# Performance work log

Hardware: AMD Instinct MI355X
Metric: run time of the kernel (lower is better)

Reference implementation:

```python
import jax, jax.numpy as jnp
import numpy as np

B, H, F, E, K = 32, 4096, 4096, 8, 2

def setup_inputs() -> dict:
    key = jax.random.key(0)
    ks = jax.random.split(key, 5)
    x = jax.random.normal(ks[0], (B, H), dtype=jnp.float32)
    Wg = jax.random.normal(ks[1], (H, E), dtype=jnp.float32) * 0.02
    W1 = jax.random.normal(ks[2], (E, H, F), dtype=jnp.float32) * 0.02
    W3 = jax.random.normal(ks[3], (E, H, F), dtype=jnp.float32) * 0.02
    W2 = jax.random.normal(ks[4], (E, F, H), dtype=jnp.float32) * 0.02
    return {"x": x, "Wg": Wg, "W1": W1, "W3": W3, "W2": W2}

def reference(x, Wg, W1, W3, W2):
    # Gate: [B, E] logits, top-2 selection, softmax over the 2 selected logits
    logits = x @ Wg                                   # [B, E]
    vals, idx = jax.lax.top_k(logits, K)              # [B, K]
    w = jax.nn.softmax(vals, axis=-1)                 # [B, K]
    # Combine weights per expert: [B, E] (zero for unselected experts)
    combine = jnp.sum(jax.nn.one_hot(idx, E, dtype=x.dtype) * w[..., None], axis=1)
    h = jnp.einsum('bh,ehf->ebf', x, W1)              # [E, B, F]
    g = jax.nn.silu(h) * jnp.einsum('bh,ehf->ebf', x, W3)
    y = jnp.einsum('ebf,efh->ebh', g, W2)             # [E, B, H]
    # Scatter-combine: weighted sum over experts (all-gather + reduce-sum in source)
    return jnp.einsum('be,ebh->bh', combine, y)       # [B, H]
```

## Files before the change

kernel.cpp:

```cpp
#include <hip/hip_runtime.h>
#include <cstdint>

#define BB 32
#define HH 4096
#define FF 4096
#define EE 8
#define NSLOT 16
#define TSEG 16
#define CH 512
#define RSTR 36

__global__ __launch_bounds__(256) void gate_kernel(const float* __restrict__ x,
                                                   const float* __restrict__ Wg,
                                                   float* __restrict__ logits) {
  int b = blockIdx.x;
  int tid = threadIdx.x;
  float acc[EE];
#pragma unroll
  for (int e = 0; e < EE; ++e) acc[e] = 0.f;
  const float* xb = x + (size_t)b * HH;
  for (int h = tid; h < HH; h += 256) {
    float xv = xb[h];
    const float4* wg = (const float4*)(Wg + (size_t)h * EE);
    float4 w0 = wg[0], w1 = wg[1];
    acc[0] = fmaf(xv, w0.x, acc[0]);
    acc[1] = fmaf(xv, w0.y, acc[1]);
    acc[2] = fmaf(xv, w0.z, acc[2]);
    acc[3] = fmaf(xv, w0.w, acc[3]);
    acc[4] = fmaf(xv, w1.x, acc[4]);
    acc[5] = fmaf(xv, w1.y, acc[5]);
    acc[6] = fmaf(xv, w1.z, acc[6]);
    acc[7] = fmaf(xv, w1.w, acc[7]);
  }
#pragma unroll
  for (int off = 32; off > 0; off >>= 1) {
#pragma unroll
    for (int e = 0; e < EE; ++e) acc[e] += __shfl_down(acc[e], off, 64);
  }
  __shared__ float part[4][EE];
  if ((tid & 63) == 0) {
#pragma unroll
    for (int e = 0; e < EE; ++e) part[tid >> 6][e] = acc[e];
  }
  __syncthreads();
  if (tid < EE) {
    logits[(size_t)b * EE + tid] =
        part[0][tid] + part[1][tid] + part[2][tid] + part[3][tid];
  }
}

__global__ void route_kernel(const float* __restrict__ logits,
                             int* __restrict__ cnt,
                             int* __restrict__ tok,
                             float* __restrict__ wts,
                             int* __restrict__ ord) {
  if (threadIdx.x != 0 || blockIdx.x != 0) return;
  int e0[BB], e1[BB];
  float p0[BB], p1[BB];
  for (int b = 0; b < BB; ++b) {
    const float* L = logits + (size_t)b * EE;
    int i0 = 0;
    float v0 = L[0];
    for (int e = 1; e < EE; ++e) {
      float v = L[e];
      if (v > v0) { v0 = v; i0 = e; }
    }
    int i1 = (i0 == 0) ? 1 : 0;
    float v1 = L[i1];
    for (int e = 0; e < EE; ++e) {
      if (e == i0) continue;
      float v = L[e];
      if (v > v1) { v1 = v; i1 = e; }
    }
    float p = 1.f / (1.f + __expf(v1 - v0));
    e0[b] = i0; e1[b] = i1; p0[b] = p; p1[b] = 1.f - p;
  }
  for (int s = 0; s < NSLOT; ++s) {
    cnt[s] = 0;
    for (int t = 0; t < TSEG; ++t) { tok[s * TSEG + t] = 0; wts[s * TSEG + t] = 0.f; }
  }
  for (int e = 0; e < EE; ++e) {
    int c = 0;
    for (int b = 0; b < BB; ++b) {
      float w = 0.f;
      int sel = 0;
      if (e0[b] == e) { w = p0[b]; sel = 1; }
      else if (e1[b] == e) { w = p1[b]; sel = 1; }
      if (sel) {
        int s = e * 2 + (c >> 4);
        int t = c & 15;
        tok[s * TSEG + t] = b;
        wts[s * TSEG + t] = w;
        cnt[s] = t + 1;
        ++c;
      }
    }
  }
  int na = 0;
  for (int s = 0; s < NSLOT; ++s) if (cnt[s] > 0) ord[na++] = s;
  for (int s = 0; s < NSLOT; ++s) if (cnt[s] == 0) ord[na++] = s;
}

__global__ __launch_bounds__(256) void buildx_kernel(const float* __restrict__ x,
                                                     const int* __restrict__ cnt,
                                                     const int* __restrict__ tok,
                                                     float* __restrict__ xseg) {
  int s = blockIdx.y;
  int c = cnt[s];
  if (c == 0) return;
  int tid = threadIdx.x;
  int t = tid & 15;
  int hoff = tid >> 4;
  int tk = tok[s * TSEG + t];
  bool act = t < c;
  int hbase = blockIdx.x * 256;
#pragma unroll
  for (int i = 0; i < 16; ++i) {
    int h = hbase + i * 16 + hoff;
    float v = act ? x[(size_t)tk * HH + h] : 0.f;
    xseg[((size_t)s * HH + h) * TSEG + t] = v;
  }
}

__device__ __forceinline__ void fma8(float4* __restrict__ acc,
                                     const float* __restrict__ xr, float4 wv) {
  float xs[8];
  *(float4*)&xs[0] = *(const float4*)(xr);
  *(float4*)&xs[4] = *(const float4*)(xr + 4);
#pragma unroll
  for (int t = 0; t < 8; ++t) {
    acc[t].x = fmaf(xs[t], wv.x, acc[t].x);
    acc[t].y = fmaf(xs[t], wv.y, acc[t].y);
    acc[t].z = fmaf(xs[t], wv.z, acc[t].z);
    acc[t].w = fmaf(xs[t], wv.w, acc[t].w);
  }
}

__device__ __forceinline__ void accum128(float4* __restrict__ acc,
                                         const float4* __restrict__ wp4,
                                         const float* __restrict__ lxw,
                                         int half8) {
  float4 ring[8];
#pragma unroll
  for (int k = 0; k < 8; ++k) ring[k] = wp4[(size_t)k * 1024];
  for (int i0 = 0; i0 + 8 < 128; i0 += 8) {
#pragma unroll
    for (int k = 0; k < 8; ++k) {
      float4 wv = ring[k];
      ring[k] = wp4[(size_t)(i0 + 8 + k) * 1024];
      fma8(acc, lxw + (i0 + k) * TSEG + half8, wv);
    }
  }
#pragma unroll
  for (int k = 0; k < 8; ++k)
    fma8(acc, lxw + (120 + k) * TSEG + half8, ring[k]);
}

__device__ __forceinline__ void stage512(float* __restrict__ lx,
                                         const float* __restrict__ src, int tid) {
  const float4* s4 = (const float4*)src;
  float4* d4 = (float4*)lx;
#pragma unroll
  for (int k = 0; k < 8; ++k) d4[k * 256 + tid] = s4[k * 256 + tid];
}

__device__ __forceinline__ void stage_silu512(float* __restrict__ lx,
                                              const float* __restrict__ h1p,
                                              const float* __restrict__ h3p, int tid) {
  const float4* a4 = (const float4*)h1p;
  const float4* b4 = (const float4*)h3p;
  float4* d4 = (float4*)lx;
#pragma unroll
  for (int k = 0; k < 8; ++k) {
    float4 a = a4[k * 256 + tid];
    float4 b = b4[k * 256 + tid];
    float4 g;
    g.x = (a.x / (1.f + __expf(-a.x))) * b.x;
    g.y = (a.y / (1.f + __expf(-a.y))) * b.y;
    g.z = (a.z / (1.f + __expf(-a.z))) * b.z;
    g.w = (a.w / (1.f + __expf(-a.w))) * b.w;
    d4[k * 256 + tid] = g;
  }
}

__device__ __forceinline__ void red_write(float* __restrict__ lds,
                                          const float4* __restrict__ acc, int tid) {
  int l = tid & 63;
  int w = tid >> 6;
  float tmp[32];
#pragma unroll
  for (int t = 0; t < 8; ++t) {
    tmp[t] = acc[t].x;
    tmp[8 + t] = acc[t].y;
    tmp[16 + t] = acc[t].z;
    tmp[24 + t] = acc[t].w;
  }
  float* rp = lds + (size_t)(w * 64 + l) * RSTR;
#pragma unroll
  for (int q = 0; q < 32; q += 4) *(float4*)(rp + q) = *(const float4*)&tmp[q];
}

__device__ __forceinline__ void red_read(const float* __restrict__ lds,
                                         float* __restrict__ v, int tid) {
  int col = tid & 127;
  int half = tid >> 7;
  int base = (half * 32 + (col >> 2)) * RSTR + (col & 3) * 8;
#pragma unroll
  for (int t = 0; t < 8; ++t) {
    float sum = 0.f;
#pragma unroll
    for (int w = 0; w < 4; ++w) sum += lds[w * 64 * RSTR + base + t];
    v[t] = sum;
  }
}

__global__ __launch_bounds__(256) void passB7_kernel(const float* __restrict__ W1,
                                                     const float* __restrict__ W3,
                                                     const float* __restrict__ xseg,
                                                     float* __restrict__ h1seg,
                                                     float* __restrict__ h3seg,
                                                     const int* __restrict__ cnt,
                                                     const int* __restrict__ ord) {
  __shared__ float lds[4 * 64 * RSTR];
  int gy = blockIdx.y;
  int s = ord[gy >> 1];
  int mat = gy & 1;
  int c = cnt[s];
  if (c == 0) return;
  int e = s >> 1;
  int tid = threadIdx.x;
  int l = tid & 63;
  int w = tid >> 6;
  int colbase = blockIdx.x * 128;
  const float* Wm = (mat ? W3 : W1) + (size_t)e * HH * FF + colbase + (l & 31) * 4;
  const float* xsrc = xseg + (size_t)s * HH * TSEG;
  int half8 = (l >> 5) * 8;
  float4 acc[8];
#pragma unroll
  for (int t = 0; t < 8; ++t) acc[t] = make_float4(0.f, 0.f, 0.f, 0.f);
  for (int ch = 0; ch < HH / CH; ++ch) {
    __syncthreads();
    stage512(lds, xsrc + (size_t)(ch * CH) * TSEG, tid);
    __syncthreads();
    const float4* wp4 = (const float4*)(Wm + (size_t)(ch * CH + w * 128) * FF);
    accum128(acc, wp4, lds + (w * 128) * TSEG, half8);
  }
  __syncthreads();
  red_write(lds, acc, tid);
  __syncthreads();
  float v[8];
  red_read(lds, v, tid);
  int col = tid & 127;
  int half = tid >> 7;
  float* seg = (mat ? h3seg : h1seg) +
               ((size_t)s * FF + colbase + col) * TSEG + half * 8;
  *(float4*)(seg) = *(const float4*)&v[0];
  *(float4*)(seg + 4) = *(const float4*)&v[4];
}

__global__ __launch_bounds__(256) void passC7_kernel(const float* __restrict__ W2,
                                                     const float* __restrict__ h1seg,
                                                     const float* __restrict__ h3seg,
                                                     const int* __restrict__ cnt,
                                                     const int* __restrict__ tok,
                                                     const float* __restrict__ wts,
                                                     const int* __restrict__ ord,
                                                     float* __restrict__ out) {
  __shared__ float lds[4 * 64 * RSTR];
  __shared__ int stok[TSEG];
  __shared__ float swt[TSEG];
  int gy = blockIdx.y;
  int s = ord[gy >> 1];
  int z = gy & 1;
  int c = cnt[s];
  if (c == 0) return;
  int e = s >> 1;
  int tid = threadIdx.x;
  int l = tid & 63;
  int w = tid >> 6;
  int colbase = blockIdx.x * 128;
  if (tid < TSEG) {
    stok[tid] = tok[s * TSEG + tid];
    swt[tid] = wts[s * TSEG + tid];
  }
  const float* Wm = W2 + (size_t)e * FF * HH + (size_t)(z * 2048) * HH +
                    colbase + (l & 31) * 4;
  const float* h1src = h1seg + ((size_t)s * FF + z * 2048) * TSEG;
  const float* h3src = h3seg + ((size_t)s * FF + z * 2048) * TSEG;
  int half8 = (l >> 5) * 8;
  float4 acc[8];
#pragma unroll
  for (int t = 0; t < 8; ++t) acc[t] = make_float4(0.f, 0.f, 0.f, 0.f);
  for (int ch = 0; ch < 4; ++ch) {
    __syncthreads();
    stage_silu512(lds, h1src + (size_t)(ch * CH) * TSEG,
                  h3src + (size_t)(ch * CH) * TSEG, tid);
    __syncthreads();
    const float4* wp4 = (const float4*)(Wm + (size_t)(ch * CH + w * 128) * HH);
    accum128(acc, wp4, lds + (w * 128) * TSEG, half8);
  }
  __syncthreads();
  red_write(lds, acc, tid);
  __syncthreads();
  float v[8];
  red_read(lds, v, tid);
  int col = tid & 127;
  int half = tid >> 7;
  float* op = out + colbase + col;
#pragma unroll
  for (int t = 0; t < 8; ++t) {
    int tt = half * 8 + t;
    if (tt < c) atomicAdd(op + (size_t)stok[tt] * HH, swt[tt] * v[t]);
  }
}

extern "C" void kernel_launch(void* const* d_in, const int* in_sizes, int n_in,
                              void* d_out, int out_size, void* d_ws, size_t ws_size,
                              hipStream_t stream) {
  const float* x  = (const float*)d_in[0];
  const float* Wg = (const float*)d_in[1];
  const float* W1 = (const float*)d_in[2];
  const float* W3 = (const float*)d_in[3];
  const float* W2 = (const float*)d_in[4];
  float* out = (float*)d_out;

  char* ws = (char*)d_ws;
  float* logits = (float*)ws;
  int*   cnt    = (int*)(ws + 1024);
  int*   tok    = (int*)(ws + 1088);
  float* wts    = (float*)(ws + 2112);
  int*   ord    = (int*)(ws + 3136);
  float* xseg   = (float*)(ws + 4096);
  float* h1seg  = xseg + (size_t)NSLOT * HH * TSEG;
  float* h3seg  = h1seg + (size_t)NSLOT * FF * TSEG;

  hipMemsetAsync(d_out, 0, (size_t)out_size * sizeof(float), stream);
  gate_kernel<<<BB, 256, 0, stream>>>(x, Wg, logits);
  route_kernel<<<1, 64, 0, stream>>>(logits, cnt, tok, wts, ord);
  buildx_kernel<<<dim3(HH / 256, NSLOT), 256, 0, stream>>>(x, cnt, tok, xseg);
  passB7_kernel<<<dim3(FF / 128, NSLOT * 2), 256, 0, stream>>>(W1, W3, xseg, h1seg, h3seg, cnt, ord);
  passC7_kernel<<<dim3(HH / 128, NSLOT * 2), 256, 0, stream>>>(W2, h1seg, h3seg, cnt, tok, wts, ord, out);
}
```

Measured before the change: 362.3 us.

## Double-buffer activation staging with async global-to-LDS loads and split SiLU

Activation chunks are now staged into LDS with global_load_lds direct copies into a double buffer, so the next chunk loads while the current one feeds the FMAs. This removes one of the two barriers per chunk. The chunk size is halved to fit two buffers, and accumulators become a flat float array. SiLU gating moves out of the W2 pass into a separate elementwise kernel that overwrites h1seg, which costs an extra launch and a pass over h1seg/h3seg in exchange for simpler staging.

```diff
diff --git a/kernel.cpp b/kernel.cpp
--- a/kernel.cpp
+++ b/kernel.cpp
@@ -7,8 +7,8 @@
 #define EE 8
 #define NSLOT 16
 #define TSEG 16
-#define CH 512
-#define RSTR 36
+#define CH 256
+#define SCR_STR 36
 
 __global__ __launch_bounds__(256) void gate_kernel(const float* __restrict__ x,
                                                    const float* __restrict__ Wg,
@@ -122,106 +122,59 @@
   }
 }
 
-__device__ __forceinline__ void fma8(float4* __restrict__ acc,
-                                     const float* __restrict__ xr, float4 wv) {
-  float xs[8];
-  *(float4*)&xs[0] = *(const float4*)(xr);
-  *(float4*)&xs[4] = *(const float4*)(xr + 4);
+__device__ __forceinline__ void stage_async(float* __restrict__ lbuf,
+                                            const float* __restrict__ src, int tid) {
+#pragma unroll
+  for (int k = 0; k < 4; ++k) {
+    int q = k * 256 + tid;
+    __builtin_amdgcn_global_load_lds(
+        (const __attribute__((address_space(1))) unsigned int*)(src + (size_t)q * 4),
+        (__attribute__((address_space(3))) unsigned int*)(lbuf + (size_t)q * 4),
+        16, 0, 0);
+  }
+}
+
+__device__ __forceinline__ void fma32(float* __restrict__ acc,
+                                      const float* __restrict__ xr, float4 wv) {
+  float4 a = *(const float4*)xr;
+  float4 b = *(const float4*)(xr + 4);
+  float xs[8] = {a.x, a.y, a.z, a.w, b.x, b.y, b.z, b.w};
 #pragma unroll
   for (int t = 0; t < 8; ++t) {
-    acc[t].x = fmaf(xs[t], wv.x, acc[t].x);
-    acc[t].y = fmaf(xs[t], wv.y, acc[t].y);
-    acc[t].z = fmaf(xs[t], wv.z, acc[t].z);
-    acc[t].w = fmaf(xs[t], wv.w, acc[t].w);
-  }
-}
-
-__device__ __forceinline__ void accum128(float4* __restrict__ acc,
-                                         const float4* __restrict__ wp4,
-                                         const float* __restrict__ lxw,
-                                         int half8) {
+    acc[t]      = fmaf(xs[t], wv.x, acc[t]);
+    acc[8 + t]  = fmaf(xs[t], wv.y, acc[8 + t]);
+    acc[16 + t] = fmaf(xs[t], wv.z, acc[16 + t]);
+    acc[24 + t] = fmaf(xs[t], wv.w, acc[24 + t]);
+  }
+}
+
+__device__ __forceinline__ void accum64(float* __restrict__ acc,
+                                        const float4* __restrict__ wp4,
+                                        const float* __restrict__ lx8) {
   float4 ring[8];
 #pragma unroll
   for (int k = 0; k < 8; ++k) ring[k] = wp4[(size_t)k * 1024];
-  for (int i0 = 0; i0 + 8 < 128; i0 += 8) {
+  for (int i0 = 0; i0 + 8 < 64; i0 += 8) {
 #pragma unroll
     for (int k = 0; k < 8; ++k) {
       float4 wv = ring[k];
       ring[k] = wp4[(size_t)(i0 + 8 + k) * 1024];
-      fma8(acc, lxw + (i0 + k) * TSEG + half8, wv);
+      fma32(acc, lx8 + (i0 + k) * TSEG, wv);
     }
   }
 #pragma unroll
   for (int k = 0; k < 8; ++k)
-    fma8(acc, lxw + (120 + k) * TSEG + half8, ring[k]);
-}
-
-__device__ __forceinline__ void stage512(float* __restrict__ lx,
-                                         const float* __restrict__ src, int tid) {
-  const float4* s4 = (const float4*)src;
-  float4* d4 = (float4*)lx;
-#pragma unroll
-  for (int k = 0; k < 8; ++k) d4[k * 256 + tid] = s4[k * 256 + tid];
-}
-
-__device__ __forceinline__ void stage_silu512(float* __restrict__ lx,
-                                              const float* __restrict__ h1p,
-                                              const float* __restrict__ h3p, int tid) {
-  const float4* a4 = (const float4*)h1p;
-  const float4* b4 = (const float4*)h3p;
-  float4* d4 = (float4*)lx;
-#pragma unroll
-  for (int k = 0; k < 8; ++k) {
-    float4 a = a4[k * 256 + tid];
-    float4 b = b4[k * 256 + tid];
-    float4 g;
-    g.x = (a.x / (1.f + __expf(-a.x))) * b.x;
-    g.y = (a.y / (1.f + __expf(-a.y))) * b.y;
-    g.z = (a.z / (1.f + __expf(-a.z))) * b.z;
-    g.w = (a.w / (1.f + __expf(-a.w))) * b.w;
-    d4[k * 256 + tid] = g;
-  }
-}
-
-__device__ __forceinline__ void red_write(float* __restrict__ lds,
-                                          const float4* __restrict__ acc, int tid) {
-  int l = tid & 63;
-  int w = tid >> 6;
-  float tmp[32];
-#pragma unroll
-  for (int t = 0; t < 8; ++t) {
-    tmp[t] = acc[t].x;
-    tmp[8 + t] = acc[t].y;
-    tmp[16 + t] = acc[t].z;
-    tmp[24 + t] = acc[t].w;
-  }
-  float* rp = lds + (size_t)(w * 64 + l) * RSTR;
-#pragma unroll
-  for (int q = 0; q < 32; q += 4) *(float4*)(rp + q) = *(const float4*)&tmp[q];
-}
-
-__device__ __forceinline__ void red_read(const float* __restrict__ lds,
-                                         float* __restrict__ v, int tid) {
-  int col = tid & 127;
-  int half = tid >> 7;
-  int base = (half * 32 + (col >> 2)) * RSTR + (col & 3) * 8;
-#pragma unroll
-  for (int t = 0; t < 8; ++t) {
-    float sum = 0.f;
-#pragma unroll
-    for (int w = 0; w < 4; ++w) sum += lds[w * 64 * RSTR + base + t];
-    v[t] = sum;
-  }
-}
-
-__global__ __launch_bounds__(256) void passB7_kernel(const float* __restrict__ W1,
-                                                     const float* __restrict__ W3,
-                                                     const float* __restrict__ xseg,
-                                                     float* __restrict__ h1seg,
-                                                     float* __restrict__ h3seg,
-                                                     const int* __restrict__ cnt,
-                                                     const int* __restrict__ ord) {
-  __shared__ float lds[4 * 64 * RSTR];
+    fma32(acc, lx8 + (56 + k) * TSEG, ring[k]);
+}
+
+__global__ __launch_bounds__(256) void passB10_kernel(const float* __restrict__ W1,
+                                                      const float* __restrict__ W3,
+                                                      const float* __restrict__ xseg,
+                                                      float* __restrict__ h1seg,
+                                                      float* __restrict__ h3seg,
+                                                      const int* __restrict__ cnt,
+                                                      const int* __restrict__ ord) {
+  __shared__ float lds[9216];
   int gy = blockIdx.y;
   int s = ord[gy >> 1];
   int mat = gy & 1;
@@ -235,38 +188,66 @@
   const float* Wm = (mat ? W3 : W1) + (size_t)e * HH * FF + colbase + (l & 31) * 4;
   const float* xsrc = xseg + (size_t)s * HH * TSEG;
   int half8 = (l >> 5) * 8;
-  float4 acc[8];
-#pragma unroll
-  for (int t = 0; t < 8; ++t) acc[t] = make_float4(0.f, 0.f, 0.f, 0.f);
+  float acc[32];
+#pragma unroll
+  for (int t = 0; t < 32; ++t) acc[t] = 0.f;
+  stage_async(lds, xsrc, tid);
+  __syncthreads();
   for (int ch = 0; ch < HH / CH; ++ch) {
+    if (ch + 1 < HH / CH)
+      stage_async(lds + ((ch + 1) & 1) * (CH * TSEG),
+                  xsrc + (size_t)(ch + 1) * CH * TSEG, tid);
+    const float4* wp4 = (const float4*)(Wm + (size_t)(ch * CH + w * 64) * FF);
+    accum64(acc, wp4, lds + (ch & 1) * (CH * TSEG) + (w * 64) * TSEG + half8);
     __syncthreads();
-    stage512(lds, xsrc + (size_t)(ch * CH) * TSEG, tid);
-    __syncthreads();
-    const float4* wp4 = (const float4*)(Wm + (size_t)(ch * CH + w * 128) * FF);
-    accum128(acc, wp4, lds + (w * 128) * TSEG, half8);
-  }
-  __syncthreads();
-  red_write(lds, acc, tid);
-  __syncthreads();
+  }
+  float* rp = lds + (size_t)(w * 64 + l) * SCR_STR;
+#pragma unroll
+  for (int q = 0; q < 32; q += 4) *(float4*)(rp + q) = *(const float4*)&acc[q];
+  __syncthreads();
+  int col_off = tid & 127;
+  int half = tid >> 7;
+  int baselane = (col_off >> 2) | (half << 5);
+  int fbase = (col_off & 3) * 8;
   float v[8];
-  red_read(lds, v, tid);
-  int col = tid & 127;
-  int half = tid >> 7;
+#pragma unroll
+  for (int j = 0; j < 8; ++j) {
+    float sum = 0.f;
+#pragma unroll
+    for (int w4 = 0; w4 < 4; ++w4)
+      sum += lds[(w4 * 64 + baselane) * SCR_STR + fbase + j];
+    v[j] = sum;
+  }
   float* seg = (mat ? h3seg : h1seg) +
-               ((size_t)s * FF + colbase + col) * TSEG + half * 8;
-  *(float4*)(seg) = *(const float4*)&v[0];
+               ((size_t)s * FF + colbase + col_off) * TSEG + half * 8;
+  *(float4*)seg = *(const float4*)&v[0];
   *(float4*)(seg + 4) = *(const float4*)&v[4];
 }
 
-__global__ __launch_bounds__(256) void passC7_kernel(const float* __restrict__ W2,
-                                                     const float* __restrict__ h1seg,
-                                                     const float* __restrict__ h3seg,
-                                                     const int* __restrict__ cnt,
-                                                     const int* __restrict__ tok,
-                                                     const float* __restrict__ wts,
-                                                     const int* __restrict__ ord,
-                                                     float* __restrict__ out) {
-  __shared__ float lds[4 * 64 * RSTR];
+__global__ __launch_bounds__(256) void silu_combine_kernel(float* __restrict__ h1seg,
+                                                           const float* __restrict__ h3seg,
+                                                           const int* __restrict__ cnt) {
+  int s = blockIdx.y;
+  if (cnt[s] == 0) return;
+  size_t i = (size_t)s * (FF * TSEG / 4) + (size_t)blockIdx.x * 256 + threadIdx.x;
+  float4 h1 = ((const float4*)h1seg)[i];
+  float4 h3 = ((const float4*)h3seg)[i];
+  float4 r;
+  r.x = (h1.x / (1.f + __expf(-h1.x))) * h3.x;
+  r.y = (h1.y / (1.f + __expf(-h1.y))) * h3.y;
+  r.z = (h1.z / (1.f + __expf(-h1.z))) * h3.z;
+  r.w = (h1.w / (1.f + __expf(-h1.w))) * h3.w;
+  ((float4*)h1seg)[i] = r;
+}
+
+__global__ __launch_bounds__(256) void passC10_kernel(const float* __restrict__ W2,
+                                                      const float* __restrict__ gseg,
+                                                      const int* __restrict__ cnt,
+                                                      const int* __restrict__ tok,
+                                                      const float* __restrict__ wts,
+                                                      const int* __restrict__ ord,
+                                                      float* __restrict__ out) {
+  __shared__ float lds[9216];
   __shared__ int stok[TSEG];
   __shared__ float swt[TSEG];
   int gy = blockIdx.y;
@@ -285,32 +266,40 @@
   }
   const float* Wm = W2 + (size_t)e * FF * HH + (size_t)(z * 2048) * HH +
                     colbase + (l & 31) * 4;
-  const float* h1src = h1seg + ((size_t)s * FF + z * 2048) * TSEG;
-  const float* h3src = h3seg + ((size_t)s * FF + z * 2048) * TSEG;
+  const float* gsrc = gseg + ((size_t)s * FF + z * 2048) * TSEG;
   int half8 = (l >> 5) * 8;
-  float4 acc[8];
-#pragma unroll
-  for (int t = 0; t < 8; ++t) acc[t] = make_float4(0.f, 0.f, 0.f, 0.f);
-  for (int ch = 0; ch < 4; ++ch) {
+  float acc[32];
+#pragma unroll
+  for (int t = 0; t < 32; ++t) acc[t] = 0.f;
+  stage_async(lds, gsrc, tid);
+  __syncthreads();
+  for (int ch = 0; ch < 2048 / CH; ++ch) {
+    if (ch + 1 < 2048 / CH)
+      stage_async(lds + ((ch + 1) & 1) * (CH * TSEG),
+                  gsrc + (size_t)(ch + 1) * CH * TSEG, tid);
+    const float4* wp4 = (const float4*)(Wm + (size_t)(ch * CH + w * 64) * HH);
+    accum64(acc, wp4, lds + (ch & 1) * (CH * TSEG) + (w * 64) * TSEG + half8);
     __syncthreads();
-    stage_silu512(lds, h1src + (size_t)(ch * CH) * TSEG,
-                  h3src + (size_t)(ch * CH) * TSEG, tid);
-    __syncthreads();
-    const float4* wp4 = (const float4*)(Wm + (size_t)(ch * CH + w * 128) * HH);
-    accum128(acc, wp4, lds + (w * 128) * TSEG, half8);
-  }
-  __syncthreads();
-  red_write(lds, acc, tid);
-  __syncthreads();
-  float v[8];
-  red_read(lds, v, tid);
-  int col = tid & 127;
+  }
+  float* rp = lds + (size_t)(w * 64 + l) * SCR_STR;
+#pragma unroll
+  for (int q = 0; q < 32; q += 4) *(float4*)(rp + q) = *(const float4*)&acc[q];
+  __syncthreads();
+  int col_off = tid & 127;
   int half = tid >> 7;
-  float* op = out + colbase + col;
-#pragma unroll
-  for (int t = 0; t < 8; ++t) {
-    int tt = half * 8 + t;
-    if (tt < c) atomicAdd(op + (size_t)stok[tt] * HH, swt[tt] * v[t]);
+  int baselane = (col_off >> 2) | (half << 5);
+  int fbase = (col_off & 3) * 8;
+  float* op = out + colbase + col_off;
+#pragma unroll
+  for (int j = 0; j < 8; ++j) {
+    int t = half * 8 + j;
+    if (t < c) {
+      float sum = 0.f;
+#pragma unroll
+      for (int w4 = 0; w4 < 4; ++w4)
+        sum += lds[(w4 * 64 + baselane) * SCR_STR + fbase + j];
+      atomicAdd(op + (size_t)stok[t] * HH, swt[t] * sum);
+    }
   }
 }
 
@@ -338,6 +327,7 @@
   gate_kernel<<<BB, 256, 0, stream>>>(x, Wg, logits);
   route_kernel<<<1, 64, 0, stream>>>(logits, cnt, tok, wts, ord);
   buildx_kernel<<<dim3(HH / 256, NSLOT), 256, 0, stream>>>(x, cnt, tok, xseg);
-  passB7_kernel<<<dim3(FF / 128, NSLOT * 2), 256, 0, stream>>>(W1, W3, xseg, h1seg, h3seg, cnt, ord);
-  passC7_kernel<<<dim3(HH / 128, NSLOT * 2), 256, 0, stream>>>(W2, h1seg, h3seg, cnt, tok, wts, ord, out);
-}
+  passB10_kernel<<<dim3(FF / 128, NSLOT * 2), 256, 0, stream>>>(W1, W3, xseg, h1seg, h3seg, cnt, ord);
+  silu_combine_kernel<<<dim3(FF * TSEG / 1024, NSLOT), 256, 0, stream>>>(h1seg, h3seg, cnt);
+  passC10_kernel<<<dim3(HH / 128, NSLOT * 2), 256, 0, stream>>>(W2, h1seg, cnt, tok, wts, ord, out);
+}
```

Result: slower. 371.7 us (+2.6%).

## Widen weight tiles to 256 columns with token-count-specialized accumulator paths

Applied to the files above, without the earlier changes.

Before, 32 lanes of a wave shared each weight float4 load and split the 16 token slots into two halves of 8. Now every lane owns a distinct column float4 and accumulates all tokens. There is an 8-accumulator path for segments with at most 8 tokens and a 16-accumulator path otherwise. This halves the grid's column blocks and removes redundant weight loads across wave halves, aiming to cut L2/VMEM traffic. In exchange, the 16-token path raises register pressure and there are fewer blocks in flight.

```diff
diff --git a/kernel.cpp b/kernel.cpp
--- a/kernel.cpp
+++ b/kernel.cpp
@@ -122,13 +122,14 @@
   }
 }
 
-__device__ __forceinline__ void fma8(float4* __restrict__ acc,
-                                     const float* __restrict__ xr, float4 wv) {
-  float xs[8];
-  *(float4*)&xs[0] = *(const float4*)(xr);
-  *(float4*)&xs[4] = *(const float4*)(xr + 4);
-#pragma unroll
-  for (int t = 0; t < 8; ++t) {
+template <int NT>
+__device__ __forceinline__ void fma_c4(float4* __restrict__ acc,
+                                       const float* __restrict__ xr, float4 wv) {
+  float xs[NT];
+#pragma unroll
+  for (int q = 0; q < NT; q += 4) *(float4*)&xs[q] = *(const float4*)(xr + q);
+#pragma unroll
+  for (int t = 0; t < NT; ++t) {
     acc[t].x = fmaf(xs[t], wv.x, acc[t].x);
     acc[t].y = fmaf(xs[t], wv.y, acc[t].y);
     acc[t].z = fmaf(xs[t], wv.z, acc[t].z);
@@ -136,10 +137,10 @@
   }
 }
 
+template <int NT>
 __device__ __forceinline__ void accum128(float4* __restrict__ acc,
                                          const float4* __restrict__ wp4,
-                                         const float* __restrict__ lxw,
-                                         int half8) {
+                                         const float* __restrict__ lxw) {
   float4 ring[8];
 #pragma unroll
   for (int k = 0; k < 8; ++k) ring[k] = wp4[(size_t)k * 1024];
@@ -148,12 +149,12 @@
     for (int k = 0; k < 8; ++k) {
       float4 wv = ring[k];
       ring[k] = wp4[(size_t)(i0 + 8 + k) * 1024];
-      fma8(acc, lxw + (i0 + k) * TSEG + half8, wv);
+      fma_c4<NT>(acc, lxw + (i0 + k) * TSEG, wv);
     }
   }
 #pragma unroll
   for (int k = 0; k < 8; ++k)
-    fma8(acc, lxw + (120 + k) * TSEG + half8, ring[k]);
+    fma_c4<NT>(acc, lxw + (120 + k) * TSEG, ring[k]);
 }
 
 __device__ __forceinline__ void stage512(float* __restrict__ lx,
@@ -183,44 +184,43 @@
   }
 }
 
-__device__ __forceinline__ void red_write(float* __restrict__ lds,
-                                          const float4* __restrict__ acc, int tid) {
+__device__ __forceinline__ void red_write8tok(float* __restrict__ lds,
+                                              const float4* __restrict__ accp,
+                                              int tid) {
   int l = tid & 63;
   int w = tid >> 6;
   float tmp[32];
 #pragma unroll
-  for (int t = 0; t < 8; ++t) {
-    tmp[t] = acc[t].x;
-    tmp[8 + t] = acc[t].y;
-    tmp[16 + t] = acc[t].z;
-    tmp[24 + t] = acc[t].w;
+  for (int j = 0; j < 8; ++j) {
+    tmp[j] = accp[j].x;
+    tmp[8 + j] = accp[j].y;
+    tmp[16 + j] = accp[j].z;
+    tmp[24 + j] = accp[j].w;
   }
   float* rp = lds + (size_t)(w * 64 + l) * RSTR;
 #pragma unroll
   for (int q = 0; q < 32; q += 4) *(float4*)(rp + q) = *(const float4*)&tmp[q];
 }
 
-__device__ __forceinline__ void red_read(const float* __restrict__ lds,
-                                         float* __restrict__ v, int tid) {
-  int col = tid & 127;
-  int half = tid >> 7;
-  int base = (half * 32 + (col >> 2)) * RSTR + (col & 3) * 8;
-#pragma unroll
-  for (int t = 0; t < 8; ++t) {
+__device__ __forceinline__ void red_read8tok(const float* __restrict__ lds,
+                                             float* __restrict__ v, int tid) {
+  int base = (tid >> 2) * RSTR + (tid & 3) * 8;
+#pragma unroll
+  for (int j = 0; j < 8; ++j) {
     float sum = 0.f;
 #pragma unroll
-    for (int w = 0; w < 4; ++w) sum += lds[w * 64 * RSTR + base + t];
-    v[t] = sum;
-  }
-}
-
-__global__ __launch_bounds__(256) void passB7_kernel(const float* __restrict__ W1,
-                                                     const float* __restrict__ W3,
-                                                     const float* __restrict__ xseg,
-                                                     float* __restrict__ h1seg,
-                                                     float* __restrict__ h3seg,
-                                                     const int* __restrict__ cnt,
-                                                     const int* __restrict__ ord) {
+    for (int w = 0; w < 4; ++w) sum += lds[w * 64 * RSTR + base + j];
+    v[j] = sum;
+  }
+}
+
+__global__ __launch_bounds__(256) void passB15_kernel(const float* __restrict__ W1,
+                                                      const float* __restrict__ W3,
+                                                      const float* __restrict__ xseg,
+                                                      float* __restrict__ h1seg,
+                                                      float* __restrict__ h3seg,
+                                                      const int* __restrict__ cnt,
+                                                      const int* __restrict__ ord) {
   __shared__ float lds[4 * 64 * RSTR];
   int gy = blockIdx.y;
   int s = ord[gy >> 1];
@@ -231,44 +231,63 @@
   int tid = threadIdx.x;
   int l = tid & 63;
   int w = tid >> 6;
-  int colbase = blockIdx.x * 128;
-  const float* Wm = (mat ? W3 : W1) + (size_t)e * HH * FF + colbase + (l & 31) * 4;
+  int colbase = blockIdx.x * 256;
+  const float* Wm = (mat ? W3 : W1) + (size_t)e * HH * FF + colbase + l * 4;
   const float* xsrc = xseg + (size_t)s * HH * TSEG;
-  int half8 = (l >> 5) * 8;
-  float4 acc[8];
-#pragma unroll
-  for (int t = 0; t < 8; ++t) acc[t] = make_float4(0.f, 0.f, 0.f, 0.f);
-  for (int ch = 0; ch < HH / CH; ++ch) {
+  float* segbase = (mat ? h3seg : h1seg) + ((size_t)s * FF + colbase) * TSEG;
+  if (c <= 8) {
+    float4 acc[8];
+#pragma unroll
+    for (int t = 0; t < 8; ++t) acc[t] = make_float4(0.f, 0.f, 0.f, 0.f);
+    for (int ch = 0; ch < HH / CH; ++ch) {
+      __syncthreads();
+      stage512(lds, xsrc + (size_t)(ch * CH) * TSEG, tid);
+      __syncthreads();
+      accum128<8>(acc, (const float4*)(Wm + (size_t)(ch * CH + w * 128) * FF),
+                  lds + (w * 128) * TSEG);
+    }
     __syncthreads();
-    stage512(lds, xsrc + (size_t)(ch * CH) * TSEG, tid);
+    red_write8tok(lds, acc, tid);
     __syncthreads();
-    const float4* wp4 = (const float4*)(Wm + (size_t)(ch * CH + w * 128) * FF);
-    accum128(acc, wp4, lds + (w * 128) * TSEG, half8);
-  }
-  __syncthreads();
-  red_write(lds, acc, tid);
-  __syncthreads();
-  float v[8];
-  red_read(lds, v, tid);
-  int col = tid & 127;
-  int half = tid >> 7;
-  float* seg = (mat ? h3seg : h1seg) +
-               ((size_t)s * FF + colbase + col) * TSEG + half * 8;
-  *(float4*)(seg) = *(const float4*)&v[0];
-  *(float4*)(seg + 4) = *(const float4*)&v[4];
-}
-
-__global__ __launch_bounds__(256) void passC7_kernel(const float* __restrict__ W2,
-                                                     const float* __restrict__ h1seg,
-                                                     const float* __restrict__ h3seg,
-                                                     const int* __restrict__ cnt,
-                                                     const int* __restrict__ tok,
-                                                     const float* __restrict__ wts,
-                                                     const int* __restrict__ ord,
-                                                     float* __restrict__ out) {
+    float v[8];
+    red_read8tok(lds, v, tid);
+    float* seg = segbase + (size_t)tid * TSEG;
+    *(float4*)(seg) = *(const float4*)&v[0];
+    *(float4*)(seg + 4) = *(const float4*)&v[4];
+  } else {
+    float4 acc[16];
+#pragma unroll
+    for (int t = 0; t < 16; ++t) acc[t] = make_float4(0.f, 0.f, 0.f, 0.f);
+    for (int ch = 0; ch < HH / CH; ++ch) {
+      __syncthreads();
+      stage512(lds, xsrc + (size_t)(ch * CH) * TSEG, tid);
+      __syncthreads();
+      accum128<16>(acc, (const float4*)(Wm + (size_t)(ch * CH + w * 128) * FF),
+                   lds + (w * 128) * TSEG);
+    }
+#pragma unroll
+    for (int p = 0; p < 2; ++p) {
+      __syncthreads();
+      red_write8tok(lds, acc + p * 8, tid);
+      __syncthreads();
+      float v[8];
+      red_read8tok(lds, v, tid);
+      float* seg = segbase + (size_t)tid * TSEG + p * 8;
+      *(float4*)(seg) = *(const float4*)&v[0];
+      *(float4*)(seg + 4) = *(const float4*)&v[4];
+    }
+  }
+}
+
+__global__ __launch_bounds__(256) void passC15_kernel(const float* __restrict__ W2,
+                                                      const float* __restrict__ h1seg,
+                                                      const float* __restrict__ h3seg,
+                                                      const int* __restrict__ cnt,
+                                                      const int* __restrict__ tok,
+                                                      const float* __restrict__ wts,
+                                                      const int* __restrict__ ord,
+                                                      float* __restrict__ out) {
   __shared__ float lds[4 * 64 * RSTR];
-  __shared__ int stok[TSEG];
-  __shared__ float swt[TSEG];
   int gy = blockIdx.y;
   int s = ord[gy >> 1];
   int z = gy & 1;
@@ -278,39 +297,61 @@
   int tid = threadIdx.x;
   int l = tid & 63;
   int w = tid >> 6;
-  int colbase = blockIdx.x * 128;
-  if (tid < TSEG) {
-    stok[tid] = tok[s * TSEG + tid];
-    swt[tid] = wts[s * TSEG + tid];
-  }
+  int colbase = blockIdx.x * 256;
   const float* Wm = W2 + (size_t)e * FF * HH + (size_t)(z * 2048) * HH +
-                    colbase + (l & 31) * 4;
+                    colbase + l * 4;
   const float* h1src = h1seg + ((size_t)s * FF + z * 2048) * TSEG;
   const float* h3src = h3seg + ((size_t)s * FF + z * 2048) * TSEG;
-  int half8 = (l >> 5) * 8;
-  float4 acc[8];
-#pragma unroll
-  for (int t = 0; t < 8; ++t) acc[t] = make_float4(0.f, 0.f, 0.f, 0.f);
-  for (int ch = 0; ch < 4; ++ch) {
+  if (c <= 8) {
+    float4 acc[8];
+#pragma unroll
+    for (int t = 0; t < 8; ++t) acc[t] = make_float4(0.f, 0.f, 0.f, 0.f);
+    for (int ch = 0; ch < 4; ++ch) {
+      __syncthreads();
+      stage_silu512(lds, h1src + (size_t)(ch * CH) * TSEG,
+                    h3src + (size_t)(ch * CH) * TSEG, tid);
+      __syncthreads();
+      accum128<8>(acc, (const float4*)(Wm + (size_t)(ch * CH + w * 128) * HH),
+                  lds + (w * 128) * TSEG);
+    }
     __syncthreads();
-    stage_silu512(lds, h1src + (size_t)(ch * CH) * TSEG,
-                  h3src + (size_t)(ch * CH) * TSEG, tid);
+    red_write8tok(lds, acc, tid);
     __syncthreads();
-    const float4* wp4 = (const float4*)(Wm + (size_t)(ch * CH + w * 128) * HH);
-    accum128(acc, wp4, lds + (w * 128) * TSEG, half8);
-  }
-  __syncthreads();
-  red_write(lds, acc, tid);
-  __syncthreads();
-  float v[8];
-  red_read(lds, v, tid);
-  int col = tid & 127;
-  int half = tid >> 7;
-  float* op = out + colbase + col;
-#pragma unroll
-  for (int t = 0; t < 8; ++t) {
-    int tt = half * 8 + t;
-    if (tt < c) atomicAdd(op + (size_t)stok[tt] * HH, swt[tt] * v[t]);
+    float v[8];
+    red_read8tok(lds, v, tid);
+    float* op = out + colbase + tid;
+#pragma unroll
+    for (int j = 0; j < 8; ++j) {
+      if (j < c) atomicAdd(op + (size_t)tok[s * TSEG + j] * HH,
+                           wts[s * TSEG + j] * v[j]);
+    }
+  } else {
+    float4 acc[16];
+#pragma unroll
+    for (int t = 0; t < 16; ++t) acc[t] = make_float4(0.f, 0.f, 0.f, 0.f);
+    for (int ch = 0; ch < 4; ++ch) {
+      __syncthreads();
+      stage_silu512(lds, h1src + (size_t)(ch * CH) * TSEG,
+                    h3src + (size_t)(ch * CH) * TSEG, tid);
+      __syncthreads();
+      accum128<16>(acc, (const float4*)(Wm + (size_t)(ch * CH + w * 128) * HH),
+                   lds + (w * 128) * TSEG);
+    }
+#pragma unroll
+    for (int p = 0; p < 2; ++p) {
+      __syncthreads();
+      red_write8tok(lds, acc + p * 8, tid);
+      __syncthreads();
+      float v[8];
+      red_read8tok(lds, v, tid);
+      float* op = out + colbase + tid;
+#pragma unroll
+      for (int j = 0; j < 8; ++j) {
+        int tt = p * 8 + j;
+        if (tt < c) atomicAdd(op + (size_t)tok[s * TSEG + tt] * HH,
+                              wts[s * TSEG + tt] * v[j]);
+      }
+    }
   }
 }
 
@@ -338,6 +379,6 @@
   gate_kernel<<<BB, 256, 0, stream>>>(x, Wg, logits);
   route_kernel<<<1, 64, 0, stream>>>(logits, cnt, tok, wts, ord);
   buildx_kernel<<<dim3(HH / 256, NSLOT), 256, 0, stream>>>(x, cnt, tok, xseg);
-  passB7_kernel<<<dim3(FF / 128, NSLOT * 2), 256, 0, stream>>>(W1, W3, xseg, h1seg, h3seg, cnt, ord);
-  passC7_kernel<<<dim3(HH / 128, NSLOT * 2), 256, 0, stream>>>(W2, h1seg, h3seg, cnt, tok, wts, ord, out);
-}
+  passB15_kernel<<<dim3(FF / 256, NSLOT * 2), 256, 0, stream>>>(W1, W3, xseg, h1seg, h3seg, cnt, ord);
+  passC15_kernel<<<dim3(HH / 256, NSLOT * 2), 256, 0, stream>>>(W2, h1seg, h3seg, cnt, tok, wts, ord, out);
+}
```

Measured after the change: 410.2 us. 1.13x slower.
